# Optimization experiments

Measured on AMD Instinct MI355X. Metric: run time of the kernel, lower is better.

Reference implementation:

```python
import jax, jax.numpy as jnp
import numpy as np

N_NODES = 16500   # 100 battles x 165 hexes
N_EDGES = 100000  # per link type
K = 3             # number of link types (HeteroConv branches)
C_IN, C_HID, C_OUT = 170, 256, 256
GEN_EPS = 1e-7    # GENConv eps
BN_EPS = 1e-5     # BatchNorm1d eps


def setup_inputs() -> dict:
    key = jax.random.key(0)
    ki = iter(jax.random.split(key, 32))
    inp = {}
    inp["x"] = jax.random.normal(next(ki), (N_NODES, C_IN), jnp.float32)
    inp["edge_index"] = jax.random.randint(next(ki), (K, 2, N_EDGES), 0, N_NODES, dtype=jnp.int32)
    inp["edge_attr"] = jax.random.normal(next(ki), (K, N_EDGES, 1), jnp.float32)

    def uni(k, fan_in, shape):
        b = float(1.0 / np.sqrt(fan_in))
        return jax.random.uniform(k, shape, jnp.float32, -b, b)

    dims = [(C_IN, C_HID), (C_HID, C_HID), (C_HID, C_OUT)]
    for l, (ci, co) in enumerate(dims):
        inp[f"We{l}"] = uni(next(ki), 1, (K, 1, ci))          # edge encoder Linear(1, ci)
        inp[f"be{l}"] = jnp.zeros((K, ci), jnp.float32)
        inp[f"Wa{l}"] = uni(next(ki), ci, (K, ci, 2 * ci))     # MLP layer 1 (expansion=2)
        inp[f"ba{l}"] = jnp.zeros((K, 2 * ci), jnp.float32)
        inp[f"g{l}"] = jnp.ones((K, 2 * ci), jnp.float32)      # BatchNorm gamma
        inp[f"bt{l}"] = jnp.zeros((K, 2 * ci), jnp.float32)    # BatchNorm beta
        inp[f"Wb{l}"] = uni(next(ki), 2 * ci, (K, 2 * ci, co)) # MLP layer 2
        inp[f"bb{l}"] = jnp.zeros((K, co), jnp.float32)
    return inp


def _genconv(x, src, dst, ea, We, be, Wa, ba, g, bt, Wb, bb):
    """PyG GENConv (aggr='softmax', t=1, eps=1e-7, norm='batch') with self loops."""
    n = x.shape[0]
    loops = jnp.arange(n, dtype=src.dtype)
    src = jnp.concatenate([src, loops])
    dst = jnp.concatenate([dst, loops])
    ea = jnp.concatenate([ea, jnp.ones((n, ea.shape[1]), ea.dtype)], axis=0)
    e = ea @ We + be                           # [E+N, ci] edge encoder
    msg = jax.nn.relu(x[src] + e) + GEN_EPS    # [E+N, ci] message
    # per-destination, per-channel segment softmax aggregation
    mx = jax.ops.segment_max(msg, dst, num_segments=n)
    w = jnp.exp(msg - mx[dst])
    den = jax.ops.segment_sum(w, dst, num_segments=n)
    aggr = jax.ops.segment_sum(msg * w, dst, num_segments=n) / den
    out = aggr + x                             # residual with root node
    # MLP: Linear -> BatchNorm(train stats) -> ReLU -> Linear
    h = out @ Wa + ba
    mu = h.mean(axis=0)
    var = ((h - mu) ** 2).mean(axis=0)
    h = (h - mu) * jax.lax.rsqrt(var + BN_EPS) * g + bt
    h = jax.nn.relu(h)
    return h @ Wb + bb


_conv_k = jax.vmap(_genconv, in_axes=(None, 0, 0, 0, 0, 0, 0, 0, 0, 0, 0, 0))


def _forward(x, edge_index, edge_attr, layers):
    h = x
    for i, p in enumerate(layers):
        # HeteroConv: run GENConv per link type, sum-aggregate over types
        h = _conv_k(h, edge_index[:, 0], edge_index[:, 1], edge_attr, *p).sum(axis=0)
        if i < len(layers) - 1:
            h = jax.nn.leaky_relu(h, 0.01)
    return h


def reference(x, edge_index, edge_attr,
              We0, be0, Wa0, ba0, g0, bt0, Wb0, bb0,
              We1, be1, Wa1, ba1, g1, bt1, Wb1, bb1,
              We2, be2, Wa2, ba2, g2, bt2, Wb2, bb2):
    layers = [(We0, be0, Wa0, ba0, g0, bt0, Wb0, bb0),
              (We1, be1, Wa1, ba1, g1, bt1, Wb1, bb1),
              (We2, be2, Wa2, ba2, g2, bt2, Wb2, bb2)]
    return _forward(x, edge_index, edge_attr, layers)
```

## Files before the change

kernel.cpp:

```cpp
#include <hip/hip_runtime.h>
#include <math.h>

#define NN 16500
#define NP 16512
#define NE 100000
#define KT 3

typedef __attribute__((ext_vector_type(8))) short bf8_t;
typedef __attribute__((ext_vector_type(4))) float f4_t;

__device__ __forceinline__ unsigned short f2bf(float f) {
    unsigned int u = __float_as_uint(f);
    u += 0x7fffu + ((u >> 16) & 1u);
    return (unsigned short)(u >> 16);
}
__device__ __forceinline__ float bf2f(unsigned short h) {
    return __uint_as_float(((unsigned int)h) << 16);
}
__device__ __forceinline__ void gload16(unsigned short* lds, const unsigned short* g) {
    __builtin_amdgcn_global_load_lds(
        (const __attribute__((address_space(1))) void*)g,
        (__attribute__((address_space(3))) void*)lds, 16, 0, 0);
}


__global__ void deg_kernel(const int* __restrict__ ei, int* __restrict__ deg) {
    int t = blockIdx.x * blockDim.x + threadIdx.x;
    if (t >= KT * NE) return;
    int k = t / NE, e = t - k * NE;
    int d = ei[k * 2 * NE + NE + e];
    atomicAdd(&deg[k * NN + d], 1);
}

__global__ void scan_kernel(const int* __restrict__ deg, int* __restrict__ offs,
                            int* __restrict__ cursor) {
    int k = blockIdx.x;
    const int* dg = deg + k * NN;
    int* of = offs + k * (NN + 1);
    int* cu = cursor + k * NN;
    __shared__ int part[256];
    int tid = threadIdx.x;
    const int chunk = (NN + 255) / 256;
    int s0 = tid * chunk, s1 = min(NN, s0 + chunk);
    if (s0 > s1) s0 = s1;
    int sum = 0;
    for (int i = s0; i < s1; ++i) sum += dg[i];
    part[tid] = sum;
    __syncthreads();
    for (int off = 1; off < 256; off <<= 1) {
        int v = part[tid];
        int vp = (tid >= off) ? part[tid - off] : 0;
        __syncthreads();
        part[tid] = v + vp;
        __syncthreads();
    }
    int run = (tid == 0) ? 0 : part[tid - 1];
    for (int i = s0; i < s1; ++i) {
        of[i] = run; cu[i] = run;
        run += dg[i];
    }
    if (tid == 255) of[NN] = run;
}

__global__ void scatter_kernel(const int* __restrict__ ei, const float* __restrict__ ea,
                               int* __restrict__ cursor, int2* __restrict__ se) {
    int t = blockIdx.x * blockDim.x + threadIdx.x;
    if (t >= KT * NE) return;
    int k = t / NE, e = t - k * NE;
    int s = ei[k * 2 * NE + e];
    int d = ei[k * 2 * NE + NE + e];
    float a = ea[(size_t)k * NE + e];
    int pos = atomicAdd(&cursor[k * NN + d], 1);
    int2 p; p.x = s; p.y = __float_as_int(a);
    se[(size_t)k * NE + pos] = p;
}


template<int CI, bool BF16X>
__device__ __forceinline__ void loadrow4(float out[4], const void* xv, int s, int c0) {
    if (BF16X) {
        const unsigned short* xb = (const unsigned short*)xv;
        uint2 u = *(const uint2*)(xb + (size_t)s * CI + c0);
        out[0] = bf2f((unsigned short)(u.x & 0xffffu));
        out[1] = bf2f((unsigned short)(u.x >> 16));
        out[2] = bf2f((unsigned short)(u.y & 0xffffu));
        out[3] = bf2f((unsigned short)(u.y >> 16));
    } else {
        const float* p = (const float*)xv + (size_t)s * CI + c0;
        if (c0 + 4 <= CI) {
            float2 ab = *(const float2*)p;
            float2 cd = *(const float2*)(p + 2);
            out[0] = ab.x; out[1] = ab.y; out[2] = cd.x; out[3] = cd.y;
        } else {
            #pragma unroll
            for (int e = 0; e < 4; ++e) out[e] = (c0 + e < CI) ? p[e] : 0.f;
        }
    }
}

template<int CI, bool BF16X>
__global__ __launch_bounds__(256) void aggr_kernel(
    const void* __restrict__ xv, const int2* __restrict__ se_all,
    const int* __restrict__ offs_all,
    const float* __restrict__ We_all, const float* __restrict__ be_all,
    unsigned short* __restrict__ out_hi)
{
    constexpr int KP = (CI + 31) / 32 * 32;
    int k = blockIdx.y;
    int wv = threadIdx.x >> 6, lane = threadIdx.x & 63;
    int c0 = lane * 4;
    unsigned short* o = out_hi + (size_t)k * NP * KP;
    const int2*  se   = se_all + (size_t)k * NE;
    const int*   offs = offs_all + k * (NN + 1);
    const float* We   = We_all + (size_t)k * CI;
    const float* be   = be_all + (size_t)k * CI;

    constexpr bool ACT_ALL = (64 * 4 == KP) && (CI == KP);
    bool act = ACT_ALL || (c0 < CI);
    float w[4], b[4];
    #pragma unroll
    for (int e = 0; e < 4; ++e) {
        bool a = (c0 + e) < CI;
        w[e] = a ? We[c0 + e] : 0.f;
        b[e] = a ? be[c0 + e] : 0.f;
    }

    for (int it = 0; it < 4; ++it) {
        int d = blockIdx.x * 16 + it * 4 + wv;
        if (d >= NN) {
            if (c0 < KP) { uint2 z = {0u, 0u}; *(uint2*)(o + (size_t)d * KP + c0) = z; }
            continue;
        }
        float xd[4] = {0.f, 0.f, 0.f, 0.f};
        if (act) loadrow4<CI, BF16X>(xd, xv, d, c0);
        #pragma unroll
        for (int e = 0; e < 4; ++e) if ((c0 + e) >= CI) xd[e] = 0.f;

        float den[4], num[4];
        #pragma unroll
        for (int e = 0; e < 4; ++e) {
            float mg = fmaxf(xd[e] + w[e] + b[e], 0.f);
            float ex = __expf(mg);
            den[e] = ex;
            num[e] = mg * ex;
        }

        auto step = [&](const float xc[4], float a) {
            #pragma unroll
            for (int e = 0; e < 4; ++e) {
                float t = xc[e] + fmaf(a, w[e], b[e]);
                float mg = fmaxf(t, 0.f);
                float ex = __expf(mg);
                den[e] += ex;
                num[e] = fmaf(mg, ex, num[e]);
            }
        };

        int start = offs[d], end = offs[d + 1];
        for (int base = start; base < end; base += 64) {
            int cnt = min(64, end - base);
            int sv = 0; float av = 0.f;
            if (lane < cnt) {
                int2 p = se[base + lane];
                sv = p.x; av = __int_as_float(p.y);
            }
            float x0[4] = {0.f,0.f,0.f,0.f}, x1[4] = {0.f,0.f,0.f,0.f};
            float x2[4] = {0.f,0.f,0.f,0.f}, x3[4] = {0.f,0.f,0.f,0.f};
            {
                int sA = __shfl(sv, 0), sB = __shfl(sv, 1);
                int sC = __shfl(sv, 2), sD = __shfl(sv, 3);
                if (act)            loadrow4<CI, BF16X>(x0, xv, sA, c0);
                if (act && cnt > 1) loadrow4<CI, BF16X>(x1, xv, sB, c0);
                if (act && cnt > 2) loadrow4<CI, BF16X>(x2, xv, sC, c0);
                if (act && cnt > 3) loadrow4<CI, BF16X>(x3, xv, sD, c0);
            }
            int j = 0;
            for (; j + 3 < cnt; j += 4) {
                float a0 = __shfl(av, j),     a1 = __shfl(av, j + 1);
                float a2 = __shfl(av, j + 2), a3 = __shfl(av, j + 3);
                int s4 = __shfl(sv, (j + 4) & 63), s5 = __shfl(sv, (j + 5) & 63);
                int s6 = __shfl(sv, (j + 6) & 63), s7 = __shfl(sv, (j + 7) & 63);
                step(x0, a0);
                if (act && (j + 4) < cnt) loadrow4<CI, BF16X>(x0, xv, s4, c0);
                step(x1, a1);
                if (act && (j + 5) < cnt) loadrow4<CI, BF16X>(x1, xv, s5, c0);
                step(x2, a2);
                if (act && (j + 6) < cnt) loadrow4<CI, BF16X>(x2, xv, s6, c0);
                step(x3, a3);
                if (act && (j + 7) < cnt) loadrow4<CI, BF16X>(x3, xv, s7, c0);
            }
            if (j < cnt)     step(x0, __shfl(av, j));
            if (j + 1 < cnt) step(x1, __shfl(av, j + 1));
            if (j + 2 < cnt) step(x2, __shfl(av, j + 2));
        }
        if (c0 < KP) {
            unsigned short r[4];
            #pragma unroll
            for (int e = 0; e < 4; ++e) {
                float v = ((c0 + e) < CI) ? (num[e] / den[e] + xd[e]) : 0.f;
                r[e] = f2bf(v);
            }
            uint2 pk = {(unsigned)r[0] | ((unsigned)r[1] << 16),
                        (unsigned)r[2] | ((unsigned)r[3] << 16)};
            *(uint2*)(o + (size_t)d * KP + c0) = pk;
        }
    }
}


struct SplitJob { const float* W; unsigned short* out; int kdim, ndim, np_, kp; };
struct SplitJobs { SplitJob j[6]; };

__global__ void split_all_kernel(SplitJobs jobs) {
    SplitJob jb = jobs.j[blockIdx.z];
    int idx = blockIdx.x * 256 + threadIdx.x;
    int total = KT * jb.np_ * jb.kp;
    if (idx >= total) return;
    int k = idx / (jb.np_ * jb.kp);
    int rem = idx - k * jb.np_ * jb.kp;
    int n = rem / jb.kp;
    int kk = rem - n * jb.kp;
    float v = (n < jb.ndim && kk < jb.kdim) ? jb.W[((size_t)k * jb.kdim + kk) * jb.ndim + n] : 0.f;
    jb.out[idx] = f2bf(v);
}


__global__ __launch_bounds__(256, 2) void gemm1_mfma(
    const unsigned short* __restrict__ A_hi,
    const unsigned short* __restrict__ B_hi,
    const float* __restrict__ bias_all, unsigned short* __restrict__ C_all,
    float* __restrict__ psum,
    int KP, int ldc, int Mv, int Nv)
{
    __shared__ unsigned short smem[16384];

    int z = blockIdx.z;
    int gxT = gridDim.x, gyT = gridDim.y;
    int NHP = gxT * 128;
    const unsigned short* Ahg = A_hi + (size_t)z * NP * KP;
    const unsigned short* Bhg = B_hi + (size_t)z * NHP * KP;
    const float* bias = bias_all + (size_t)z * Nv;
    unsigned short* C = C_all + (size_t)z * NP * ldc;

    int tid = threadIdx.x;
    int w = tid >> 6, l = tid & 63;
    int bm = blockIdx.y * 128, bn = blockIdx.x * 128;
    int lane15 = l & 15, quad = l >> 4;
    int wm = (w >> 1) * 64, wn = (w & 1) * 64;
    int srow = l & 15;
    int scol = (l >> 4) * 8;

    f4_t acc[4][4];
    #pragma unroll
    for (int i = 0; i < 4; ++i)
        #pragma unroll
        for (int j = 0; j < 4; ++j) { f4_t zz = {0.f,0.f,0.f,0.f}; acc[i][j] = zz; }

    size_t aoff0 = (size_t)(bm + 32 * w +  0 + srow) * KP + scol;
    size_t aoff1 = (size_t)(bm + 32 * w + 16 + srow) * KP + scol;
    size_t boff0 = (size_t)(bn + 32 * w +  0 + srow) * KP + scol;
    size_t boff1 = (size_t)(bn + 32 * w + 16 + srow) * KP + scol;
    int rb0 = 32 * w, rb1 = 32 * w + 16;
    int ta = (w >> 1) * 4, tb = (w & 1) * 4;

    gload16(&smem[0 + rb0 * 32], Ahg + aoff0);
    gload16(&smem[0 + rb1 * 32], Ahg + aoff1);
    gload16(&smem[8192 + rb0 * 32], Bhg + boff0);
    gload16(&smem[8192 + rb1 * 32], Bhg + boff1);
    __syncthreads();

    int curo = 0;
    for (int k0 = 32; k0 < KP; k0 += 32) {
        int nxto = curo ^ 4096;
        gload16(&smem[nxto + rb0 * 32], Ahg + aoff0 + k0);
        gload16(&smem[nxto + rb1 * 32], Ahg + aoff1 + k0);
        gload16(&smem[8192 + nxto + rb0 * 32], Bhg + boff0 + k0);
        gload16(&smem[8192 + nxto + rb1 * 32], Bhg + boff1 + k0);

        bf8_t fa[4], fb[4];
        #pragma unroll
        for (int i = 0; i < 4; ++i) {
            fa[i] = *(const bf8_t*)&smem[curo + (ta + i) * 512 + l * 8];
            fb[i] = *(const bf8_t*)&smem[8192 + curo + (tb + i) * 512 + l * 8];
        }
        #pragma unroll
        for (int i = 0; i < 4; ++i)
            #pragma unroll
            for (int j = 0; j < 4; ++j)
                acc[i][j] = __builtin_amdgcn_mfma_f32_16x16x32_bf16(fa[i], fb[j], acc[i][j], 0, 0, 0);
        __syncthreads();
        curo = nxto;
    }
    {
        bf8_t fa[4], fb[4];
        #pragma unroll
        for (int i = 0; i < 4; ++i) {
            fa[i] = *(const bf8_t*)&smem[curo + (ta + i) * 512 + l * 8];
            fb[i] = *(const bf8_t*)&smem[8192 + curo + (tb + i) * 512 + l * 8];
        }
        #pragma unroll
        for (int i = 0; i < 4; ++i)
            #pragma unroll
            for (int j = 0; j < 4; ++j)
                acc[i][j] = __builtin_amdgcn_mfma_f32_16x16x32_bf16(fa[i], fb[j], acc[i][j], 0, 0, 0);
    }

    __syncthreads();

    #pragma unroll
    for (int j = 0; j < 4; ++j) {
        int c = bn + wn + j * 16 + lane15;
        float bc = (c < Nv) ? bias[c] : 0.f;
        float s1 = 0.f, s2 = 0.f;
        #pragma unroll
        for (int i = 0; i < 4; ++i) {
            #pragma unroll
            for (int r5 = 0; r5 < 4; ++r5) {
                int r = bm + wm + i * 16 + quad * 4 + r5;
                float v = acc[i][j][r5] + bc;
                unsigned short q = f2bf(v);
                int lr = wm + i * 16 + quad * 4 + r5;
                int lc = wn + j * 16 + lane15;
                smem[lr * 128 + lc] = q;
                bool ok = (r < NN) && (c < Nv);
                float vq = ok ? bf2f(q) : 0.f;
                s1 += vq;
                s2 = fmaf(vq, vq, s2);
            }
        }
        s1 += __shfl_xor(s1, 16); s2 += __shfl_xor(s2, 16);
        s1 += __shfl_xor(s1, 32); s2 += __shfl_xor(s2, 32);
        if (quad == 0) {
            int wrow = w >> 1;
            int col = wn + j * 16 + lane15;
            size_t o = ((((size_t)z * gyT + blockIdx.y) * gxT + blockIdx.x) * 2 + wrow) * 256 + col * 2;
            float2 st = {s1, s2};
            *(float2*)&psum[o] = st;
        }
    }
    __syncthreads();

    int lr8 = tid >> 4;
    int lc8 = (tid & 15) * 8;
    bool cok = (bn + lc8 + 8) <= ldc;
    if (cok) {
        #pragma unroll
        for (int p = 0; p < 8; ++p) {
            int row = p * 16 + lr8;
            uint4 v = *(const uint4*)&smem[row * 128 + lc8];
            *(uint4*)&C[(size_t)(bm + row) * ldc + bn + lc8] = v;
        }
    }
}


__global__ __launch_bounds__(256) void finalize_kernel(
    const float* __restrict__ psum,
    const float* __restrict__ g_all, const float* __restrict__ bt_all,
    float* __restrict__ scale_all, float* __restrict__ shift_all,
    int hid, int gxT)
{
    int z = blockIdx.x;
    int t64 = threadIdx.x & 63;
    int slice = threadIdx.x >> 6;
    int c = blockIdx.y * 64 + t64;
    __shared__ double rs1[4][64];
    __shared__ double rs2[4][64];
    double s1 = 0.0, s2 = 0.0;
    if (c < gxT * 128) {
        int gx = c >> 7, col = c & 127;
        for (int gy = slice; gy < NP / 128; gy += 4) {
            size_t base = (((size_t)z * (NP / 128) + gy) * gxT + gx) * 2 * 256 + col * 2;
            float2 a  = *(const float2*)&psum[base];
            float2 b2 = *(const float2*)&psum[base + 256];
            s1 += (double)a.x + b2.x;
            s2 += (double)a.y + b2.y;
        }
    }
    rs1[slice][t64] = s1;
    rs2[slice][t64] = s2;
    __syncthreads();
    if (slice == 0 && c < hid) {
        double S1 = rs1[0][t64] + rs1[1][t64] + rs1[2][t64] + rs1[3][t64];
        double S2 = rs2[0][t64] + rs2[1][t64] + rs2[2][t64] + rs2[3][t64];
        double mu = S1 / NN;
        double var = S2 / NN - mu * mu;
        if (var < 0.0) var = 0.0;
        float rs = (float)(1.0 / sqrt(var + 1e-5));
        float sc = rs * g_all[(size_t)z * hid + c];
        scale_all[(size_t)z * 512 + c] = sc;
        shift_all[(size_t)z * 512 + c] = bt_all[(size_t)z * hid + c] - (float)mu * sc;
    }
}


__global__ __launch_bounds__(256, 2) void gemm2_mfma(
    const unsigned short* __restrict__ h_all, const float* __restrict__ scale_all,
    const float* __restrict__ shift_all,
    const unsigned short* __restrict__ B_hi,
    const float* __restrict__ bb,
    float* __restrict__ outf, unsigned short* __restrict__ outb,
    int KP, int hid, int leaky, int as_bf16)
{
    __shared__ unsigned short Ah[2][64 * 32];
    __shared__ unsigned short Bh[2][128 * 32];
    __shared__ float sclS[KT * 512];
    __shared__ float shfS[KT * 512];

    int tid = threadIdx.x;
    int w = tid >> 6, l = tid & 63;
    int bm = blockIdx.y * 64, bn = blockIdx.x * 128;
    int lane15 = l & 15, quad = l >> 4;
    int wm = (w >> 1) * 32, wn = (w & 1) * 64;
    int srow = l & 15, scol = (l >> 4) * 8;

    const int KPZ = KP / 32;
    const int NIT = 3 * KPZ;

    f4_t acc[2][4];
    #pragma unroll
    for (int i = 0; i < 2; ++i)
        #pragma unroll
        for (int j = 0; j < 4; ++j) { f4_t zz = {0.f,0.f,0.f,0.f}; acc[i][j] = zz; }

    int rb0 = 32 * w, rb1 = 32 * w + 16;
    int ta = (w >> 1) * 2, tb = (w & 1) * 4;
    int grow = 16 * w + lane15;
    int ccol = quad * 8;

    size_t arow  = (size_t)(bm + grow) * KP + ccol;
    size_t brow0 = (size_t)(bn + 32 * w + srow) * KP + scol;
    size_t brow1 = (size_t)(bn + 32 * w + 16 + srow) * KP + scol;

    for (int idx = tid; idx < KT * 512; idx += 256) {
        sclS[idx] = scale_all[idx];
        shfS[idx] = shift_all[idx];
    }
    gload16(&Ah[0][tid * 8], h_all + arow);
    gload16(&Bh[0][rb0 * 32], B_hi + brow0);
    gload16(&Bh[0][rb1 * 32], B_hi + brow1);
    __syncthreads();

    int cur = 0;
    for (int it = 0; it < NIT; ++it) {
        int nit = it + 1;
        int nxt = cur ^ 1;
        if (nit < NIT) {
            int nzz = nit / KPZ, nkk = (nit - nzz * KPZ) * 32;
            const unsigned short* hz = h_all + (size_t)nzz * NP * KP + nkk;
            const unsigned short* bz = B_hi + (size_t)nzz * 256 * KP + nkk;
            gload16(&Ah[nxt][tid * 8], hz + arow);
            gload16(&Bh[nxt][rb0 * 32], bz + brow0);
            gload16(&Bh[nxt][rb1 * 32], bz + brow1);
        }
        int zz = it / KPZ, kk = (it - zz * KPZ) * 32;
        int chb = kk + quad * 8;
        float4 s0 = *(const float4*)&sclS[zz * 512 + chb];
        float4 s1 = *(const float4*)&sclS[zz * 512 + chb + 4];
        float4 t0 = *(const float4*)&shfS[zz * 512 + chb];
        float4 t1 = *(const float4*)&shfS[zz * 512 + chb + 4];
        float ss[8] = {s0.x, s0.y, s0.z, s0.w, s1.x, s1.y, s1.z, s1.w};
        float tt[8] = {t0.x, t0.y, t0.z, t0.w, t1.x, t1.y, t1.z, t1.w};
        bf8_t fr0 = *(const bf8_t*)&Ah[cur][(ta + 0) * 512 + l * 8];
        bf8_t fr1 = *(const bf8_t*)&Ah[cur][(ta + 1) * 512 + l * 8];
        bf8_t fb[4];
        #pragma unroll
        for (int j = 0; j < 4; ++j)
            fb[j] = *(const bf8_t*)&Bh[cur][(tb + j) * 512 + l * 8];
        bf8_t fa0, fa1;
        #pragma unroll
        for (int e = 0; e < 8; ++e) {
            bool okc = (chb + e) < hid;
            float x0 = bf2f((unsigned short)fr0[e]);
            float x1 = bf2f((unsigned short)fr1[e]);
            float v0 = okc ? fmaxf(fmaf(x0, ss[e], tt[e]), 0.f) : 0.f;
            float v1 = okc ? fmaxf(fmaf(x1, ss[e], tt[e]), 0.f) : 0.f;
            fa0[e] = (short)f2bf(v0);
            fa1[e] = (short)f2bf(v1);
        }
        #pragma unroll
        for (int j = 0; j < 4; ++j) {
            acc[0][j] = __builtin_amdgcn_mfma_f32_16x16x32_bf16(fa0, fb[j], acc[0][j], 0, 0, 0);
            acc[1][j] = __builtin_amdgcn_mfma_f32_16x16x32_bf16(fa1, fb[j], acc[1][j], 0, 0, 0);
        }
        __syncthreads();
        cur = nxt;
    }

    #pragma unroll
    for (int j = 0; j < 4; ++j) {
        int c = bn + wn + j * 16 + lane15;
        float bsum = bb[c] + bb[256 + c] + bb[512 + c];
        #pragma unroll
        for (int i = 0; i < 2; ++i) {
            #pragma unroll
            for (int r5 = 0; r5 < 4; ++r5) {
                int r = bm + wm + i * 16 + quad * 4 + r5;
                if (r < NN) {
                    float v = acc[i][j][r5] + bsum;
                    if (leaky) v = (v > 0.f) ? v : 0.01f * v;
                    if (as_bf16) outb[(size_t)r * 256 + c] = f2bf(v);
                    else         outf[(size_t)r * 256 + c] = v;
                }
            }
        }
    }
}


extern "C" void kernel_launch(void* const* d_in, const int* in_sizes, int n_in,
                              void* d_out, int out_size, void* d_ws, size_t ws_size,
                              hipStream_t stream)
{
    const float* x  = (const float*)d_in[0];
    const int*   ei = (const int*)d_in[1];
    const float* ea = (const float*)d_in[2];

    char* w = (char*)d_ws;
    auto alloc = [&](size_t bytes) {
        char* p = w;
        w += (bytes + 255) & ~(size_t)255;
        return p;
    };
    int* deg    = (int*)alloc((size_t)KT * NN * 4);
    int* offs   = (int*)alloc((size_t)KT * (NN + 1) * 4);
    int* cursor = (int*)alloc((size_t)KT * NN * 4);
    int2* se    = (int2*)alloc((size_t)KT * NE * 8);
    unsigned short* a1_hi = (unsigned short*)alloc((size_t)KT * NP * 256 * 2);
    unsigned short* h3 = (unsigned short*)alloc((size_t)KT * NP * 512 * 2);
    unsigned short* bta_l[3];
    unsigned short* btb_l[3];
    for (int l = 0; l < 3; ++l) {
        bta_l[l] = (unsigned short*)alloc((size_t)KT * 512 * 256 * 2);
        btb_l[l] = (unsigned short*)alloc((size_t)KT * 256 * 512 * 2);
    }
    float* psum = (float*)alloc((size_t)KT * (NP / 128) * 4 * 2 * 256 * 4);
    float* scale3 = (float*)alloc((size_t)KT * 512 * 4);
    float* shift3 = (float*)alloc((size_t)KT * 512 * 4);
    unsigned short* bufA = (unsigned short*)alloc((size_t)NN * 256 * 2);
    unsigned short* bufB = (unsigned short*)alloc((size_t)NN * 256 * 2);

    (void)hipMemsetAsync(deg, 0, (size_t)KT * NN * 4, stream);
    int net = KT * NE;
    deg_kernel<<<(net + 255) / 256, 256, 0, stream>>>(ei, deg);
    scan_kernel<<<KT, 256, 0, stream>>>(deg, offs, cursor);
    scatter_kernel<<<(net + 255) / 256, 256, 0, stream>>>(ei, ea, cursor, se);

    SplitJobs jobs;
    int maxtot = 0;
    for (int l = 0; l < 3; ++l) {
        int ci  = (l == 0) ? 170 : 256;
        int KP1 = (ci + 31) / 32 * 32;
        int hid = 2 * ci;
        int NHP = (hid + 127) / 128 * 128;
        int KP2 = (hid + 31) / 32 * 32;
        jobs.j[2 * l]     = { (const float*)d_in[3 + 8 * l + 2], bta_l[l], ci,  hid, NHP, KP1 };
        jobs.j[2 * l + 1] = { (const float*)d_in[3 + 8 * l + 6], btb_l[l], hid, 256, 256, KP2 };
        maxtot = max(maxtot, KT * NHP * KP1);
        maxtot = max(maxtot, KT * 256 * KP2);
    }
    dim3 gsp((maxtot + 255) / 256, 1, 6);
    split_all_kernel<<<gsp, 256, 0, stream>>>(jobs);

    const void* hin = x;
    for (int l = 0; l < 3; ++l) {
        int ci  = (l == 0) ? 170 : 256;
        int KP1 = (ci + 31) / 32 * 32;
        int hid = 2 * ci;
        int NHP = (hid + 127) / 128 * 128;
        int KP2 = (hid + 31) / 32 * 32;
        const float* We = (const float*)d_in[3 + 8 * l + 0];
        const float* be = (const float*)d_in[3 + 8 * l + 1];
        const float* ba = (const float*)d_in[3 + 8 * l + 3];
        const float* g  = (const float*)d_in[3 + 8 * l + 4];
        const float* bt = (const float*)d_in[3 + 8 * l + 5];
        const float* bb = (const float*)d_in[3 + 8 * l + 7];

        dim3 ga(NP / 16, KT);
        if (l == 0)
            aggr_kernel<170, false><<<ga, 256, 0, stream>>>(hin, se, offs, We, be, a1_hi);
        else
            aggr_kernel<256, true><<<ga, 256, 0, stream>>>(hin, se, offs, We, be, a1_hi);

        dim3 g1(NHP / 128, NP / 128, KT);
        gemm1_mfma<<<g1, 256, 0, stream>>>(a1_hi, bta_l[l], ba, h3, psum, KP1, KP2, NN, hid);

        dim3 gf(KT, 8);
        finalize_kernel<<<gf, 256, 0, stream>>>(psum, g, bt, scale3, shift3, hid, NHP / 128);

        unsigned short* outb = (l == 0) ? bufA : bufB;
        dim3 g2(2, NP / 64);
        gemm2_mfma<<<g2, 256, 0, stream>>>(h3, scale3, shift3, btb_l[l], bb,
                                           (float*)d_out, outb, KP2, hid,
                                           (l < 2) ? 1 : 0, (l < 2) ? 1 : 0);

        hin = (l < 2) ? (const void*)outb : nullptr;
    }
}
```

Measured before the change: 649.0 us.

## Retile gemm2 to 64x64 blocks with 64-deep K steps and higher occupancy

```diff
diff --git a/kernel.cpp b/kernel.cpp
--- a/kernel.cpp
+++ b/kernel.cpp
@@ -394,7 +394,7 @@
 }
 
 
-__global__ __launch_bounds__(256, 2) void gemm2_mfma(
+__global__ __launch_bounds__(256, 4) void gemm2_mfma(
     const unsigned short* __restrict__ h_all, const float* __restrict__ scale_all,
     const float* __restrict__ shift_all,
     const unsigned short* __restrict__ B_hi,
@@ -402,86 +402,72 @@
     float* __restrict__ outf, unsigned short* __restrict__ outb,
     int KP, int hid, int leaky, int as_bf16)
 {
-    __shared__ unsigned short Ah[2][64 * 32];
-    __shared__ unsigned short Bh[2][128 * 32];
-    __shared__ float sclS[KT * 512];
-    __shared__ float shfS[KT * 512];
+    __shared__ unsigned short Ah[2][4096];
+    __shared__ unsigned short Bh[2][4096];
 
     int tid = threadIdx.x;
     int w = tid >> 6, l = tid & 63;
-    int bm = blockIdx.y * 64, bn = blockIdx.x * 128;
+    int bm = blockIdx.y * 64, bn = blockIdx.x * 64;
     int lane15 = l & 15, quad = l >> 4;
-    int wm = (w >> 1) * 32, wn = (w & 1) * 64;
-    int srow = l & 15, scol = (l >> 4) * 8;
-
-    const int KPZ = KP / 32;
+
+    const int KPZ = KP / 64;
     const int NIT = 3 * KPZ;
 
-    f4_t acc[2][4];
+    f4_t acc[4];
     #pragma unroll
-    for (int i = 0; i < 2; ++i)
-        #pragma unroll
-        for (int j = 0; j < 4; ++j) { f4_t zz = {0.f,0.f,0.f,0.f}; acc[i][j] = zz; }
-
-    int rb0 = 32 * w, rb1 = 32 * w + 16;
-    int ta = (w >> 1) * 2, tb = (w & 1) * 4;
-    int grow = 16 * w + lane15;
-    int ccol = quad * 8;
-
-    size_t arow  = (size_t)(bm + grow) * KP + ccol;
-    size_t brow0 = (size_t)(bn + 32 * w + srow) * KP + scol;
-    size_t brow1 = (size_t)(bn + 32 * w + 16 + srow) * KP + scol;
-
-    for (int idx = tid; idx < KT * 512; idx += 256) {
-        sclS[idx] = scale_all[idx];
-        shfS[idx] = shift_all[idx];
-    }
-    gload16(&Ah[0][tid * 8], h_all + arow);
-    gload16(&Bh[0][rb0 * 32], B_hi + brow0);
-    gload16(&Bh[0][rb1 * 32], B_hi + brow1);
+    for (int j = 0; j < 4; ++j) { f4_t zz = {0.f,0.f,0.f,0.f}; acc[j] = zz; }
+
+    size_t arow = (size_t)(bm + 16 * w + lane15) * KP + quad * 8;
+    int adst0 = (0 * 4 + w) * 512, adst1 = (1 * 4 + w) * 512;
+    int fb0 = 2 * w, fb1 = 2 * w + 1;
+    size_t brow0 = (size_t)(bn + 16 * (fb0 & 3) + lane15) * KP + (fb0 >> 2) * 32 + quad * 8;
+    size_t brow1 = (size_t)(bn + 16 * (fb1 & 3) + lane15) * KP + (fb1 >> 2) * 32 + quad * 8;
+    int bdst0 = fb0 * 512, bdst1 = fb1 * 512;
+
+    gload16(&Ah[0][adst0 + l * 8], h_all + arow);
+    gload16(&Ah[0][adst1 + l * 8], h_all + arow + 32);
+    gload16(&Bh[0][bdst0 + l * 8], B_hi + brow0);
+    gload16(&Bh[0][bdst1 + l * 8], B_hi + brow1);
     __syncthreads();
 
     int cur = 0;
     for (int it = 0; it < NIT; ++it) {
-        int nit = it + 1;
-        int nxt = cur ^ 1;
+        int nit = it + 1, nxt = cur ^ 1;
         if (nit < NIT) {
-            int nzz = nit / KPZ, nkk = (nit - nzz * KPZ) * 32;
+            int nzz = nit / KPZ, nkk = (nit - nzz * KPZ) * 64;
             const unsigned short* hz = h_all + (size_t)nzz * NP * KP + nkk;
             const unsigned short* bz = B_hi + (size_t)nzz * 256 * KP + nkk;
-            gload16(&Ah[nxt][tid * 8], hz + arow);
-            gload16(&Bh[nxt][rb0 * 32], bz + brow0);
-            gload16(&Bh[nxt][rb1 * 32], bz + brow1);
-        }
-        int zz = it / KPZ, kk = (it - zz * KPZ) * 32;
-        int chb = kk + quad * 8;
-        float4 s0 = *(const float4*)&sclS[zz * 512 + chb];
-        float4 s1 = *(const float4*)&sclS[zz * 512 + chb + 4];
-        float4 t0 = *(const float4*)&shfS[zz * 512 + chb];
-        float4 t1 = *(const float4*)&shfS[zz * 512 + chb + 4];
-        float ss[8] = {s0.x, s0.y, s0.z, s0.w, s1.x, s1.y, s1.z, s1.w};
-        float tt[8] = {t0.x, t0.y, t0.z, t0.w, t1.x, t1.y, t1.z, t1.w};
-        bf8_t fr0 = *(const bf8_t*)&Ah[cur][(ta + 0) * 512 + l * 8];
-        bf8_t fr1 = *(const bf8_t*)&Ah[cur][(ta + 1) * 512 + l * 8];
-        bf8_t fb[4];
-        #pragma unroll
-        for (int j = 0; j < 4; ++j)
-            fb[j] = *(const bf8_t*)&Bh[cur][(tb + j) * 512 + l * 8];
-        bf8_t fa0, fa1;
-        #pragma unroll
-        for (int e = 0; e < 8; ++e) {
-            bool okc = (chb + e) < hid;
-            float x0 = bf2f((unsigned short)fr0[e]);
-            float x1 = bf2f((unsigned short)fr1[e]);
-            float v0 = okc ? fmaxf(fmaf(x0, ss[e], tt[e]), 0.f) : 0.f;
-            float v1 = okc ? fmaxf(fmaf(x1, ss[e], tt[e]), 0.f) : 0.f;
-            fa0[e] = (short)f2bf(v0);
-            fa1[e] = (short)f2bf(v1);
-        }
-        #pragma unroll
-        for (int j = 0; j < 4; ++j) {
-            acc[0][j] = __builtin_amdgcn_mfma_f32_16x16x32_bf16(fa0, fb[j], acc[0][j], 0, 0, 0);
-            acc[1][j] = __builtin_amdgcn_mfma_f32_16x16x32_bf16(fa1, fb[j], acc[1][j], 0, 0, 0);
+            gload16(&Ah[nxt][adst0 + l * 8], hz + arow);
+            gload16(&Ah[nxt][adst1 + l * 8], hz + arow + 32);
+            gload16(&Bh[nxt][bdst0 + l * 8], bz + brow0);
+            gload16(&Bh[nxt][bdst1 + l * 8], bz + brow1);
+        }
+        int zz = it / KPZ, kk = (it - zz * KPZ) * 64;
+        #pragma unroll
+        for (int ks = 0; ks < 2; ++ks) {
+            int chb = kk + ks * 32 + quad * 8;
+            const float* scl = scale_all + zz * 512 + chb;
+            const float* shf = shift_all + zz * 512 + chb;
+            float4 s0 = *(const float4*)scl, s1 = *(const float4*)(scl + 4);
+            float4 t0 = *(const float4*)shf, t1 = *(const float4*)(shf + 4);
+            float ss[8] = {s0.x, s0.y, s0.z, s0.w, s1.x, s1.y, s1.z, s1.w};
+            float tt[8] = {t0.x, t0.y, t0.z, t0.w, t1.x, t1.y, t1.z, t1.w};
+            bf8_t fr = *(const bf8_t*)&Ah[cur][(ks * 4 + w) * 512 + l * 8];
+            bf8_t fa;
+            #pragma unroll
+            for (int e = 0; e < 8; ++e) {
+                bool okc = (chb + e) < hid;
+                float x = bf2f((unsigned short)fr[e]);
+                float v = okc ? fmaxf(fmaf(x, ss[e], tt[e]), 0.f) : 0.f;
+                fa[e] = (short)f2bf(v);
+            }
+            bf8_t fbv[4];
+            #pragma unroll
+            for (int j = 0; j < 4; ++j)
+                fbv[j] = *(const bf8_t*)&Bh[cur][(ks * 4 + j) * 512 + l * 8];
+            #pragma unroll
+            for (int j = 0; j < 4; ++j)
+                acc[j] = __builtin_amdgcn_mfma_f32_16x16x32_bf16(fa, fbv[j], acc[j], 0, 0, 0);
         }
         __syncthreads();
         cur = nxt;
@@ -489,19 +475,16 @@
 
     #pragma unroll
     for (int j = 0; j < 4; ++j) {
-        int c = bn + wn + j * 16 + lane15;
+        int c = bn + j * 16 + lane15;
         float bsum = bb[c] + bb[256 + c] + bb[512 + c];
         #pragma unroll
-        for (int i = 0; i < 2; ++i) {
-            #pragma unroll
-            for (int r5 = 0; r5 < 4; ++r5) {
-                int r = bm + wm + i * 16 + quad * 4 + r5;
-                if (r < NN) {
-                    float v = acc[i][j][r5] + bsum;
-                    if (leaky) v = (v > 0.f) ? v : 0.01f * v;
-                    if (as_bf16) outb[(size_t)r * 256 + c] = f2bf(v);
-                    else         outf[(size_t)r * 256 + c] = v;
-                }
+        for (int r5 = 0; r5 < 4; ++r5) {
+            int r = bm + 16 * w + quad * 4 + r5;
+            if (r < NN) {
+                float v = acc[j][r5] + bsum;
+                if (leaky) v = (v > 0.f) ? v : 0.01f * v;
+                if (as_bf16) outb[(size_t)r * 256 + c] = f2bf(v);
+                else         outf[(size_t)r * 256 + c] = v;
             }
         }
     }
@@ -553,7 +536,7 @@
         int KP1 = (ci + 31) / 32 * 32;
         int hid = 2 * ci;
         int NHP = (hid + 127) / 128 * 128;
-        int KP2 = (hid + 31) / 32 * 32;
+        int KP2 = (hid + 63) / 64 * 64;
         jobs.j[2 * l]     = { (const float*)d_in[3 + 8 * l + 2], bta_l[l], ci,  hid, NHP, KP1 };
         jobs.j[2 * l + 1] = { (const float*)d_in[3 + 8 * l + 6], btb_l[l], hid, 256, 256, KP2 };
         maxtot = max(maxtot, KT * NHP * KP1);
@@ -568,7 +551,7 @@
         int KP1 = (ci + 31) / 32 * 32;
         int hid = 2 * ci;
         int NHP = (hid + 127) / 128 * 128;
-        int KP2 = (hid + 31) / 32 * 32;
+        int KP2 = (hid + 63) / 64 * 64;
         const float* We = (const float*)d_in[3 + 8 * l + 0];
         const float* be = (const float*)d_in[3 + 8 * l + 1];
         const float* ba = (const float*)d_in[3 + 8 * l + 3];
@@ -589,7 +572,7 @@
         finalize_kernel<<<gf, 256, 0, stream>>>(psum, g, bt, scale3, shift3, hid, NHP / 128);
 
         unsigned short* outb = (l == 0) ? bufA : bufB;
-        dim3 g2(2, NP / 64);
+        dim3 g2(4, NP / 64);
         gemm2_mfma<<<g2, 256, 0, stream>>>(h3, scale3, shift3, btb_l[l], bb,
                                            (float*)d_out, outb, KP2, hid,
                                            (l < 2) ? 1 : 0, (l < 2) ? 1 : 0);
```

Result: slower. 757.1 us (+16.7%).
